# Performance work log

Measured on AMD Instinct MI355X. Metric: run time of the kernel, lower is better.

## Reference

```python
import jax, jax.numpy as jnp
import numpy as np

NEG_INF = -1e6  # d2l masked_softmax mask value

def setup_inputs() -> dict:
    key = jax.random.key(0)
    ks = jax.random.split(key, 6)
    B, Lq, Lk, dq, dv, H = 8, 256, 512, 256, 256, 64
    return {
        "queries": jax.random.normal(ks[0], (B, Lq, dq), jnp.float32),
        "keys": jax.random.normal(ks[1], (B, Lk, dq), jnp.float32),
        "values": jax.random.normal(ks[2], (B, Lk, dv), jnp.float32),
        "valid_lens": jax.random.randint(ks[3], (B,), 0, Lk),
        "W_q": jax.random.normal(ks[4], (H, dq), jnp.float32) * (dq ** -0.5),
        "W_k": jax.random.normal(ks[5], (H, dq), jnp.float32) * (dq ** -0.5),
        "w_v": jax.random.normal(jax.random.fold_in(key, 7), (H,), jnp.float32) * (H ** -0.5),
    }

def reference(queries, keys, values, valid_lens, W_q, W_k, w_v):
    # Project: [B,Lq,H], [B,Lk,H]
    q = jnp.einsum('bqd,hd->bqh', queries, W_q)
    k = jnp.einsum('bkd,hd->bkh', keys, W_k)
    # Broadcast-add + tanh: [B,Lq,Lk,H]
    features = jnp.tanh(q[:, :, None, :] + k[:, None, :, :])
    # Scalar projection -> scores [B,Lq,Lk]
    scores = jnp.einsum('bqkh,h->bqk', features, w_v)
    # masked_softmax over last axis with per-batch valid_lens
    Lk = keys.shape[1]
    mask = jnp.arange(Lk)[None, None, :] < valid_lens[:, None, None]
    scores = jnp.where(mask, scores, NEG_INF)
    attn = jax.nn.softmax(scores, axis=-1)
    # dropout p=0 (inference) -> identity; bmm with values
    return jnp.einsum('bqk,bkv->bqv', attn, values)
```

## Files before the change

### kernel.cpp

```cpp
#include <hip/hip_runtime.h>
#include <hip/hip_bf16.h>
#include <hip/hip_fp16.h>
#include <stdint.h>

#define NB 8
#define LQ 256
#define LK 512
#define NH 64
#define SCALE 2.8853900817779268f
#define L2E 1.4426950408889634f

#define QP_OFF   0
#define KP_OFF   131072
#define VBF_OFF  393216
#define PL_OFF   917504

extern "C" __device__ float __ocml_exp2_f32(float);
static __device__ __forceinline__ float fexp2(float x) {
#if __has_builtin(__builtin_amdgcn_exp2f)
  return __builtin_amdgcn_exp2f(x);
#else
  return __ocml_exp2_f32(x);
#endif
}
static __device__ __forceinline__ float frcp(float x) {
  return __builtin_amdgcn_rcpf(x);
}
static __device__ __forceinline__ uint16_t f2bf(float f) {
  uint32_t u = __float_as_uint(f);
  uint32_t r = (u + 0x7FFFu + ((u >> 16) & 1u)) >> 16;
  return (uint16_t)r;
}

typedef const __attribute__((address_space(1))) void* gas_ptr;
typedef __attribute__((address_space(3))) void* las_ptr;
static __device__ __forceinline__ void gload16(const void* g, void* l) {
  __builtin_amdgcn_global_load_lds((gas_ptr)g, (las_ptr)l, 16, 0, 0);
}

__global__ __launch_bounds__(256) void proj_kernel(
    const float* __restrict__ queries, const float* __restrict__ keys,
    const float* __restrict__ values,
    const float* __restrict__ Wq, const float* __restrict__ Wk,
    float* __restrict__ qp, float* __restrict__ kp, uint16_t* __restrict__ vbf)
{
  __shared__ float Wt[256][36];
  const int blk = blockIdx.x;
  const int t = threadIdx.x;

  if (blk >= 192) {
    int base = (blk - 192) * 16384 + t * 4;
#pragma unroll
    for (int it = 0; it < 16; ++it) {
      int idx = base + it * 1024;
      float4 v = *(const float4*)(values + idx);
      uint32_t lo = (uint32_t)f2bf(v.x) | ((uint32_t)f2bf(v.y) << 16);
      uint32_t hi = (uint32_t)f2bf(v.z) | ((uint32_t)f2bf(v.w) << 16);
      uint2 pk = {lo, hi};
      *(uint2*)(vbf + idx) = pk;
    }
    return;
  }

  const bool isQ = (blk < 64);
  const int sub = isQ ? blk : (blk - 64);
  const int tile = sub >> 1;
  const int hh = (sub & 1) * 32;
  const int rowbase = tile * 64;
  const float* __restrict__ X = isQ ? queries : keys;
  const float* __restrict__ W = isQ ? Wq : Wk;
  float* __restrict__ P = isQ ? qp : kp;

#pragma unroll 4
  for (int it = 0; it < 32; ++it) {
    Wt[t][it] = W[(hh + it) * 256 + t];
  }
  __syncthreads();

  const int ty = t >> 3;
  const int tx = t & 7;
  float a0x = 0.f, a0y = 0.f, a0z = 0.f, a0w = 0.f;
  float a1x = 0.f, a1y = 0.f, a1z = 0.f, a1w = 0.f;

  const float* xr0 = X + (size_t)(rowbase + ty * 2) * 256;
  const float* xr1 = xr0 + 256;

#pragma unroll 4
  for (int d4 = 0; d4 < 64; ++d4) {
    int d = d4 * 4;
    float4 x0 = *(const float4*)(xr0 + d);
    float4 x1 = *(const float4*)(xr1 + d);
    float4 w0 = *(const float4*)&Wt[d + 0][tx * 4];
    float4 w1 = *(const float4*)&Wt[d + 1][tx * 4];
    float4 w2 = *(const float4*)&Wt[d + 2][tx * 4];
    float4 w3 = *(const float4*)&Wt[d + 3][tx * 4];
#define STEP(XC, WD) \
    a0x = fmaf(x0.XC, WD.x, a0x); a0y = fmaf(x0.XC, WD.y, a0y); \
    a0z = fmaf(x0.XC, WD.z, a0z); a0w = fmaf(x0.XC, WD.w, a0w); \
    a1x = fmaf(x1.XC, WD.x, a1x); a1y = fmaf(x1.XC, WD.y, a1y); \
    a1z = fmaf(x1.XC, WD.z, a1z); a1w = fmaf(x1.XC, WD.w, a1w);
    STEP(x, w0) STEP(y, w1) STEP(z, w2) STEP(w, w3)
#undef STEP
  }

  {
    int row0 = rowbase + ty * 2;
    int h = hh + tx * 4;
    float4 o0 = {a0x * SCALE, a0y * SCALE, a0z * SCALE, a0w * SCALE};
    float4 o1 = {a1x * SCALE, a1y * SCALE, a1z * SCALE, a1w * SCALE};
    *(float4*)&P[(size_t)row0 * 64 + h] = o0;
    *(float4*)&P[(size_t)(row0 + 1) * 64 + h] = o1;
  }
}

__global__ __launch_bounds__(256) void attn_kernel(
    const float* __restrict__ qp, const float* __restrict__ kp,
    const uint16_t* __restrict__ vbf, const float* __restrict__ w_v,
    const int* __restrict__ valid_lens, float* __restrict__ out,
    float* __restrict__ pl, float* __restrict__ pacc, int nsplit)
{
  __shared__ float kTs[32][64];
  __shared__ uint16_t Vs[32][256];
  __shared__ float p_s[4][2][32];

  const int t = threadIdx.x;
  const int lane = t & 63;
  const int w = t >> 6;
  const int r2 = lane >> 5;
  const int kx = lane & 31;
  const int wg = blockIdx.x;
  const int b = wg & 7;
  const int qg = (wg >> 3) & 31;
  const int kh = wg >> 8;
  const int row = b * LQ + qg * 8 + w * 2 + r2;

  const int vl = valid_lens[b];
  const int n = (vl > 0) ? vl : LK;
  const int span = LK / nsplit;
  const int kstart = kh * span;
  int cnt = n - kstart;
  if (cnt > span) cnt = span;
  const int ntiles = (cnt > 0) ? ((cnt + 31) >> 5) : 0;

  if (ntiles == 0) {
    if (kx == 0) pl[row * nsplit + kh] = 0.f;
    float4 z = {0.f, 0.f, 0.f, 0.f};
    float* pa = pacc + ((size_t)(row * nsplit + kh)) * 256 + kx * 8;
    *(float4*)(pa + 0) = z;
    *(float4*)(pa + 4) = z;
    return;
  }

  const float* kpb = kp + (size_t)(b * LK) * 64;
  const char* vbc = (const char*)(vbf + (size_t)b * LK * 256);

#define STAGE(K0) do { \
    int i0 = w * 2; \
    int kjr0 = i0 * 4 + (lane >> 4); \
    int cph = lane & 15; \
    gload16(kpb + (size_t)((K0) + kjr0) * 64 + (cph ^ (kjr0 & 7)) * 4, \
            &kTs[i0 * 4][0]); \
    int kjr1 = kjr0 + 4; \
    gload16(kpb + (size_t)((K0) + kjr1) * 64 + (cph ^ (kjr1 & 7)) * 4, \
            &kTs[i0 * 4 + 4][0]); \
    const char* vsrc = vbc + (size_t)(K0) * 512 + (size_t)w * 4096 + lane * 16; \
    gload16(vsrc + 0 * 1024, &Vs[w * 8 + 0][0]); \
    gload16(vsrc + 1 * 1024, &Vs[w * 8 + 2][0]); \
    gload16(vsrc + 2 * 1024, &Vs[w * 8 + 4][0]); \
    gload16(vsrc + 3 * 1024, &Vs[w * 8 + 6][0]); \
  } while (0)

  STAGE(kstart);

  float W1 = 0.f;
#pragma unroll
  for (int g = 0; g < 16; ++g) {
    float4 wf = *(const float4*)(w_v + g * 4);
    W1 += (wf.x + wf.y) + (wf.z + wf.w);
  }
  const float W1L = W1 * L2E;

  float qv[64];
  {
    const float* qrow = qp + (size_t)row * 64;
#pragma unroll
    for (int i = 0; i < 16; ++i) {
      float4 v = *(const float4*)(qrow + i * 4);
      qv[i * 4 + 0] = v.x; qv[i * 4 + 1] = v.y;
      qv[i * 4 + 2] = v.z; qv[i * 4 + 3] = v.w;
    }
  }

  float l = 0.f;
  float acc[16];
#pragma unroll
  for (int i = 0; i < 16; ++i) acc[i] = 0.f;

  for (int tt = 0; tt < ntiles; ++tt) {
    const int k0 = kstart + tt * 32;
    asm volatile("s_waitcnt vmcnt(0)" ::: "memory");
    __builtin_amdgcn_sched_barrier(0);
    __builtin_amdgcn_s_barrier();
    __builtin_amdgcn_sched_barrier(0);
    __builtin_amdgcn_s_setprio(1);

    float r0 = 0.f, r1 = 0.f, r2a = 0.f, r3 = 0.f;
#pragma unroll
    for (int g = 0; g < 16; ++g) {
      float4 kf = *(const float4*)&kTs[kx][((g ^ (kx & 7)) << 2)];
      float4 wf = *(const float4*)(w_v + g * 4);
      r0  = fmaf(wf.x, frcp(1.f + fexp2(qv[g * 4 + 0] + kf.x)), r0);
      r1  = fmaf(wf.y, frcp(1.f + fexp2(qv[g * 4 + 1] + kf.y)), r1);
      r2a = fmaf(wf.z, frcp(1.f + fexp2(qv[g * 4 + 2] + kf.z)), r2a);
      r3  = fmaf(wf.w, frcp(1.f + fexp2(qv[g * 4 + 3] + kf.w)), r3);
    }
    float racc = (r0 + r1) + (r2a + r3);

    float pe = fexp2(fmaf(-SCALE, racc, W1L));
    int kg = k0 + kx;
    float p;
    if (vl == 0)      p = 1.f;
    else if (kg < n)  p = pe;
    else              p = 0.f;

    l += p;
    p_s[w][r2][kx] = p;

    const int c = kx;
#pragma unroll
    for (int i4 = 0; i4 < 4; ++i4) {
      float4 p0 = *(const float4*)&p_s[w][0][r2 * 16 + i4 * 4];
      float4 p1 = *(const float4*)&p_s[w][1][r2 * 16 + i4 * 4];
#pragma unroll
      for (int jj = 0; jj < 4; ++jj) {
        int kk = r2 * 16 + i4 * 4 + jj;
        uint4 vv = *(const uint4*)&Vs[kk][c * 8];
        float pj0 = (jj == 0) ? p0.x : (jj == 1) ? p0.y : (jj == 2) ? p0.z : p0.w;
        float pj1 = (jj == 0) ? p1.x : (jj == 1) ? p1.y : (jj == 2) ? p1.z : p1.w;
        float f0 = __uint_as_float(vv.x << 16);
        float f1 = __uint_as_float(vv.x & 0xFFFF0000u);
        float f2 = __uint_as_float(vv.y << 16);
        float f3 = __uint_as_float(vv.y & 0xFFFF0000u);
        float f4 = __uint_as_float(vv.z << 16);
        float f5 = __uint_as_float(vv.z & 0xFFFF0000u);
        float f6 = __uint_as_float(vv.w << 16);
        float f7 = __uint_as_float(vv.w & 0xFFFF0000u);
        acc[0] = fmaf(pj0, f0, acc[0]);   acc[8]  = fmaf(pj1, f0, acc[8]);
        acc[1] = fmaf(pj0, f1, acc[1]);   acc[9]  = fmaf(pj1, f1, acc[9]);
        acc[2] = fmaf(pj0, f2, acc[2]);   acc[10] = fmaf(pj1, f2, acc[10]);
        acc[3] = fmaf(pj0, f3, acc[3]);   acc[11] = fmaf(pj1, f3, acc[11]);
        acc[4] = fmaf(pj0, f4, acc[4]);   acc[12] = fmaf(pj1, f4, acc[12]);
        acc[5] = fmaf(pj0, f5, acc[5]);   acc[13] = fmaf(pj1, f5, acc[13]);
        acc[6] = fmaf(pj0, f6, acc[6]);   acc[14] = fmaf(pj1, f6, acc[14]);
        acc[7] = fmaf(pj0, f7, acc[7]);   acc[15] = fmaf(pj1, f7, acc[15]);
      }
    }
    __builtin_amdgcn_s_setprio(0);
    __builtin_amdgcn_sched_barrier(0);
    __builtin_amdgcn_s_barrier();
    if (tt + 1 < ntiles) STAGE(k0 + 32);
  }
#undef STAGE

#pragma unroll
  for (int i = 0; i < 16; ++i) acc[i] += __shfl_xor(acc[i], 32, 64);
#pragma unroll
  for (int s = 16; s; s >>= 1) l += __shfl_xor(l, s, 64);

  const float* accr = acc + r2 * 8;
  if (nsplit == 1) {
    float inv = 1.f / l;
    float4 o0 = {accr[0] * inv, accr[1] * inv, accr[2] * inv, accr[3] * inv};
    float4 o1 = {accr[4] * inv, accr[5] * inv, accr[6] * inv, accr[7] * inv};
    float* op = out + (size_t)row * 256 + kx * 8;
    *(float4*)(op + 0) = o0;
    *(float4*)(op + 4) = o1;
  } else {
    if (kx == 0) pl[row * nsplit + kh] = l;
    float* pa = pacc + ((size_t)(row * nsplit + kh)) * 256 + kx * 8;
    float4 a0 = {accr[0], accr[1], accr[2], accr[3]};
    float4 a1 = {accr[4], accr[5], accr[6], accr[7]};
    *(float4*)(pa + 0) = a0;
    *(float4*)(pa + 4) = a1;
  }
}

__global__ __launch_bounds__(256) void merge_kernel(
    const float* __restrict__ pl, const float* __restrict__ pacc,
    float* __restrict__ out, int nsplit)
{
  const int t = threadIdx.x;
  const int row = blockIdx.x * 8 + (t >> 5);
  const int d8 = t & 31;

  float L = 0.f;
  float o[8];
#pragma unroll
  for (int i = 0; i < 8; ++i) o[i] = 0.f;

  for (int kh = 0; kh < nsplit; ++kh) {
    L += pl[row * nsplit + kh];
    const float* pa = pacc + ((size_t)(row * nsplit + kh)) * 256 + d8 * 8;
    float4 a0 = *(const float4*)(pa + 0);
    float4 a1 = *(const float4*)(pa + 4);
    o[0] += a0.x; o[1] += a0.y; o[2] += a0.z; o[3] += a0.w;
    o[4] += a1.x; o[5] += a1.y; o[6] += a1.z; o[7] += a1.w;
  }
  float inv = 1.f / L;
  float4 o0 = {o[0] * inv, o[1] * inv, o[2] * inv, o[3] * inv};
  float4 o1 = {o[4] * inv, o[5] * inv, o[6] * inv, o[7] * inv};
  float* op = out + (size_t)row * 256 + d8 * 8;
  *(float4*)(op + 0) = o0;
  *(float4*)(op + 4) = o1;
}

extern "C" void kernel_launch(void* const* d_in, const int* in_sizes, int n_in,
                              void* d_out, int out_size, void* d_ws, size_t ws_size,
                              hipStream_t stream) {
  const float* queries    = (const float*)d_in[0];
  const float* keys       = (const float*)d_in[1];
  const float* values     = (const float*)d_in[2];
  const int*   valid_lens = (const int*)d_in[3];
  const float* Wq         = (const float*)d_in[4];
  const float* Wk         = (const float*)d_in[5];
  const float* w_v        = (const float*)d_in[6];
  float* out = (float*)d_out;

  float* ws = (float*)d_ws;
  float* qp  = ws + QP_OFF;
  float* kp  = ws + KP_OFF;
  uint16_t* vbf = (uint16_t*)(ws + VBF_OFF);
  float* pl  = ws + PL_OFF;

  int nsplit;
  if      (ws_size >= (size_t)PL_OFF * 4 + 2048u * 4 * 4 + 2048u * 4 * 1024) nsplit = 4;
  else if (ws_size >= (size_t)PL_OFF * 4 + 2048u * 2 * 4 + 2048u * 2 * 1024) nsplit = 2;
  else nsplit = 1;
  float* pacc = pl + (size_t)2048 * nsplit;

  hipLaunchKernelGGL(proj_kernel, dim3(256), dim3(256), 0, stream,
                     queries, keys, values, Wq, Wk, qp, kp, vbf);
  hipLaunchKernelGGL(attn_kernel, dim3(nsplit * 256), dim3(256), 0, stream,
                     qp, kp, vbf, w_v, valid_lens, out, pl, pacc, nsplit);
  if (nsplit > 1) {
    hipLaunchKernelGGL(merge_kernel, dim3(256), dim3(256), 0, stream,
                       pl, pacc, out, nsplit);
  }
}
```

Measured before the change: 44.34 us.

## Move query rows to LDS, halve accumulators, raise occupancy and allow 8-way split

Each lane no longer keeps the 64-float projected query row in registers. The block stages its 8 query rows in shared memory once and reads a float4 per step of the score loop. The PV accumulation changes so each lane handles its own query row over all 32 keys with 8 accumulators. That removes the cross-half shuffle reduction and halves the accumulator registers. A launch bound of 8 blocks per CU and an 8-way key split, used when the workspace is large enough, add occupancy and parallelism, at the cost of extra LDS reads of V and query data plus a heavier merge pass.

```diff
diff --git a/kernel.cpp b/kernel.cpp
--- a/kernel.cpp
+++ b/kernel.cpp
@@ -113,7 +113,7 @@
   }
 }
 
-__global__ __launch_bounds__(256) void attn_kernel(
+__global__ __launch_bounds__(256, 8) void attn_kernel(
     const float* __restrict__ qp, const float* __restrict__ kp,
     const uint16_t* __restrict__ vbf, const float* __restrict__ w_v,
     const int* __restrict__ valid_lens, float* __restrict__ out,
@@ -121,6 +121,7 @@
 {
   __shared__ float kTs[32][64];
   __shared__ uint16_t Vs[32][256];
+  __shared__ float q_s[4][2][64];
   __shared__ float p_s[4][2][32];
 
   const int t = threadIdx.x;
@@ -172,6 +173,11 @@
 
   STAGE(kstart);
 
+  {
+    const float2* qsrc = (const float2*)(qp + (size_t)(b * LQ + qg * 8) * 64);
+    ((float2*)q_s)[t] = qsrc[t];
+  }
+
   float W1 = 0.f;
 #pragma unroll
   for (int g = 0; g < 16; ++g) {
@@ -180,21 +186,10 @@
   }
   const float W1L = W1 * L2E;
 
-  float qv[64];
-  {
-    const float* qrow = qp + (size_t)row * 64;
-#pragma unroll
-    for (int i = 0; i < 16; ++i) {
-      float4 v = *(const float4*)(qrow + i * 4);
-      qv[i * 4 + 0] = v.x; qv[i * 4 + 1] = v.y;
-      qv[i * 4 + 2] = v.z; qv[i * 4 + 3] = v.w;
-    }
-  }
-
   float l = 0.f;
-  float acc[16];
-#pragma unroll
-  for (int i = 0; i < 16; ++i) acc[i] = 0.f;
+  float acc[8];
+#pragma unroll
+  for (int i = 0; i < 8; ++i) acc[i] = 0.f;
 
   for (int tt = 0; tt < ntiles; ++tt) {
     const int k0 = kstart + tt * 32;
@@ -208,11 +203,12 @@
 #pragma unroll
     for (int g = 0; g < 16; ++g) {
       float4 kf = *(const float4*)&kTs[kx][((g ^ (kx & 7)) << 2)];
+      float4 qf = *(const float4*)&q_s[w][r2][g * 4];
       float4 wf = *(const float4*)(w_v + g * 4);
-      r0  = fmaf(wf.x, frcp(1.f + fexp2(qv[g * 4 + 0] + kf.x)), r0);
-      r1  = fmaf(wf.y, frcp(1.f + fexp2(qv[g * 4 + 1] + kf.y)), r1);
-      r2a = fmaf(wf.z, frcp(1.f + fexp2(qv[g * 4 + 2] + kf.z)), r2a);
-      r3  = fmaf(wf.w, frcp(1.f + fexp2(qv[g * 4 + 3] + kf.w)), r3);
+      r0  = fmaf(wf.x, frcp(1.f + fexp2(qf.x + kf.x)), r0);
+      r1  = fmaf(wf.y, frcp(1.f + fexp2(qf.y + kf.y)), r1);
+      r2a = fmaf(wf.z, frcp(1.f + fexp2(qf.z + kf.z)), r2a);
+      r3  = fmaf(wf.w, frcp(1.f + fexp2(qf.w + kf.w)), r3);
     }
     float racc = (r0 + r1) + (r2a + r3);
 
@@ -228,15 +224,13 @@
 
     const int c = kx;
 #pragma unroll
-    for (int i4 = 0; i4 < 4; ++i4) {
-      float4 p0 = *(const float4*)&p_s[w][0][r2 * 16 + i4 * 4];
-      float4 p1 = *(const float4*)&p_s[w][1][r2 * 16 + i4 * 4];
+    for (int kk4 = 0; kk4 < 8; ++kk4) {
+      float4 pf = *(const float4*)&p_s[w][r2][kk4 * 4];
 #pragma unroll
       for (int jj = 0; jj < 4; ++jj) {
-        int kk = r2 * 16 + i4 * 4 + jj;
+        int kk = kk4 * 4 + jj;
         uint4 vv = *(const uint4*)&Vs[kk][c * 8];
-        float pj0 = (jj == 0) ? p0.x : (jj == 1) ? p0.y : (jj == 2) ? p0.z : p0.w;
-        float pj1 = (jj == 0) ? p1.x : (jj == 1) ? p1.y : (jj == 2) ? p1.z : p1.w;
+        float pj = (jj == 0) ? pf.x : (jj == 1) ? pf.y : (jj == 2) ? pf.z : pf.w;
         float f0 = __uint_as_float(vv.x << 16);
         float f1 = __uint_as_float(vv.x & 0xFFFF0000u);
         float f2 = __uint_as_float(vv.y << 16);
@@ -245,14 +239,14 @@
         float f5 = __uint_as_float(vv.z & 0xFFFF0000u);
         float f6 = __uint_as_float(vv.w << 16);
         float f7 = __uint_as_float(vv.w & 0xFFFF0000u);
-        acc[0] = fmaf(pj0, f0, acc[0]);   acc[8]  = fmaf(pj1, f0, acc[8]);
-        acc[1] = fmaf(pj0, f1, acc[1]);   acc[9]  = fmaf(pj1, f1, acc[9]);
-        acc[2] = fmaf(pj0, f2, acc[2]);   acc[10] = fmaf(pj1, f2, acc[10]);
-        acc[3] = fmaf(pj0, f3, acc[3]);   acc[11] = fmaf(pj1, f3, acc[11]);
-        acc[4] = fmaf(pj0, f4, acc[4]);   acc[12] = fmaf(pj1, f4, acc[12]);
-        acc[5] = fmaf(pj0, f5, acc[5]);   acc[13] = fmaf(pj1, f5, acc[13]);
-        acc[6] = fmaf(pj0, f6, acc[6]);   acc[14] = fmaf(pj1, f6, acc[14]);
-        acc[7] = fmaf(pj0, f7, acc[7]);   acc[15] = fmaf(pj1, f7, acc[15]);
+        acc[0] = fmaf(pj, f0, acc[0]);
+        acc[1] = fmaf(pj, f1, acc[1]);
+        acc[2] = fmaf(pj, f2, acc[2]);
+        acc[3] = fmaf(pj, f3, acc[3]);
+        acc[4] = fmaf(pj, f4, acc[4]);
+        acc[5] = fmaf(pj, f5, acc[5]);
+        acc[6] = fmaf(pj, f6, acc[6]);
+        acc[7] = fmaf(pj, f7, acc[7]);
       }
     }
     __builtin_amdgcn_s_setprio(0);
@@ -263,23 +257,20 @@
 #undef STAGE
 
 #pragma unroll
-  for (int i = 0; i < 16; ++i) acc[i] += __shfl_xor(acc[i], 32, 64);
-#pragma unroll
   for (int s = 16; s; s >>= 1) l += __shfl_xor(l, s, 64);
 
-  const float* accr = acc + r2 * 8;
   if (nsplit == 1) {
     float inv = 1.f / l;
-    float4 o0 = {accr[0] * inv, accr[1] * inv, accr[2] * inv, accr[3] * inv};
-    float4 o1 = {accr[4] * inv, accr[5] * inv, accr[6] * inv, accr[7] * inv};
+    float4 o0 = {acc[0] * inv, acc[1] * inv, acc[2] * inv, acc[3] * inv};
+    float4 o1 = {acc[4] * inv, acc[5] * inv, acc[6] * inv, acc[7] * inv};
     float* op = out + (size_t)row * 256 + kx * 8;
     *(float4*)(op + 0) = o0;
     *(float4*)(op + 4) = o1;
   } else {
     if (kx == 0) pl[row * nsplit + kh] = l;
     float* pa = pacc + ((size_t)(row * nsplit + kh)) * 256 + kx * 8;
-    float4 a0 = {accr[0], accr[1], accr[2], accr[3]};
-    float4 a1 = {accr[4], accr[5], accr[6], accr[7]};
+    float4 a0 = {acc[0], acc[1], acc[2], acc[3]};
+    float4 a1 = {acc[4], acc[5], acc[6], acc[7]};
     *(float4*)(pa + 0) = a0;
     *(float4*)(pa + 4) = a1;
   }
@@ -333,7 +324,8 @@
   float* pl  = ws + PL_OFF;
 
   int nsplit;
-  if      (ws_size >= (size_t)PL_OFF * 4 + 2048u * 4 * 4 + 2048u * 4 * 1024) nsplit = 4;
+  if      (ws_size >= (size_t)PL_OFF * 4 + 2048u * 8 * 4 + 2048u * 8 * 1024) nsplit = 8;
+  else if (ws_size >= (size_t)PL_OFF * 4 + 2048u * 4 * 4 + 2048u * 4 * 1024) nsplit = 4;
   else if (ws_size >= (size_t)PL_OFF * 4 + 2048u * 2 * 4 + 2048u * 2 * 1024) nsplit = 2;
   else nsplit = 1;
   float* pacc = pl + (size_t)2048 * nsplit;
```

After: 51.78 us. 16.8% more time.

## Give each lane its own key and loop over two query rows per wave

Applied to the files above, without the earlier changes.

The score phase now maps one key per lane over a 64-key tile, and each lane evaluates both query rows of the wave in sequence, with the query rows staged in shared memory instead of held in 64 registers. Key and value tiles double to 64 rows. The split-K count drops from 4 to 2, so the split-K partial writes and merge traffic shrink. The aim is to free registers and to use all 64 lanes in the tanh phase. The cost is fewer workgroups (512 instead of 1024), larger shared memory per block, and extra LDS reads of the query rows.

```diff
diff --git a/kernel.cpp b/kernel.cpp
--- a/kernel.cpp
+++ b/kernel.cpp
@@ -119,20 +119,22 @@
     const int* __restrict__ valid_lens, float* __restrict__ out,
     float* __restrict__ pl, float* __restrict__ pacc, int nsplit)
 {
-  __shared__ float kTs[32][64];
-  __shared__ uint16_t Vs[32][256];
-  __shared__ float p_s[4][2][32];
+  __shared__ float kTs[64][64];
+  __shared__ uint16_t Vs[64][256];
+  __shared__ float q_s[4][2][64];
+  __shared__ float p_s[4][2][64];
 
   const int t = threadIdx.x;
   const int lane = t & 63;
   const int w = t >> 6;
-  const int r2 = lane >> 5;
-  const int kx = lane & 31;
+  const int half = lane >> 5;
+  const int c = lane & 31;
+  const int kj = lane;
   const int wg = blockIdx.x;
   const int b = wg & 7;
   const int qg = (wg >> 3) & 31;
   const int kh = wg >> 8;
-  const int row = b * LQ + qg * 8 + w * 2 + r2;
+  const int row0 = b * LQ + qg * 8 + w * 2;
 
   const int vl = valid_lens[b];
   const int n = (vl > 0) ? vl : LK;
@@ -140,12 +142,12 @@
   const int kstart = kh * span;
   int cnt = n - kstart;
   if (cnt > span) cnt = span;
-  const int ntiles = (cnt > 0) ? ((cnt + 31) >> 5) : 0;
+  const int ntiles = (cnt > 0) ? ((cnt + 63) >> 6) : 0;
 
   if (ntiles == 0) {
-    if (kx == 0) pl[row * nsplit + kh] = 0.f;
+    if (c == 0) pl[(row0 + half) * nsplit + kh] = 0.f;
     float4 z = {0.f, 0.f, 0.f, 0.f};
-    float* pa = pacc + ((size_t)(row * nsplit + kh)) * 256 + kx * 8;
+    float* pa = pacc + ((size_t)((row0 + half) * nsplit + kh)) * 256 + c * 8;
     *(float4*)(pa + 0) = z;
     *(float4*)(pa + 4) = z;
     return;
@@ -155,22 +157,37 @@
   const char* vbc = (const char*)(vbf + (size_t)b * LK * 256);
 
 #define STAGE(K0) do { \
-    int i0 = w * 2; \
-    int kjr0 = i0 * 4 + (lane >> 4); \
     int cph = lane & 15; \
-    gload16(kpb + (size_t)((K0) + kjr0) * 64 + (cph ^ (kjr0 & 7)) * 4, \
-            &kTs[i0 * 4][0]); \
-    int kjr1 = kjr0 + 4; \
-    gload16(kpb + (size_t)((K0) + kjr1) * 64 + (cph ^ (kjr1 & 7)) * 4, \
-            &kTs[i0 * 4 + 4][0]); \
-    const char* vsrc = vbc + (size_t)(K0) * 512 + (size_t)w * 4096 + lane * 16; \
-    gload16(vsrc + 0 * 1024, &Vs[w * 8 + 0][0]); \
-    gload16(vsrc + 1 * 1024, &Vs[w * 8 + 2][0]); \
-    gload16(vsrc + 2 * 1024, &Vs[w * 8 + 4][0]); \
-    gload16(vsrc + 3 * 1024, &Vs[w * 8 + 6][0]); \
+    int kr0 = w * 16 + (lane >> 4); \
+    gload16(kpb + (size_t)((K0) + kr0) * 64 + ((cph ^ (kr0 & 7)) << 2), \
+            &kTs[w * 16][0]); \
+    int kr1 = kr0 + 4; \
+    gload16(kpb + (size_t)((K0) + kr1) * 64 + ((cph ^ (kr1 & 7)) << 2), \
+            &kTs[w * 16 + 4][0]); \
+    int kr2 = kr0 + 8; \
+    gload16(kpb + (size_t)((K0) + kr2) * 64 + ((cph ^ (kr2 & 7)) << 2), \
+            &kTs[w * 16 + 8][0]); \
+    int kr3 = kr0 + 12; \
+    gload16(kpb + (size_t)((K0) + kr3) * 64 + ((cph ^ (kr3 & 7)) << 2), \
+            &kTs[w * 16 + 12][0]); \
+    const char* vsrc = vbc + (size_t)((K0) + w * 16) * 512 + lane * 16; \
+    gload16(vsrc + 0 * 1024, &Vs[w * 16 +  0][0]); \
+    gload16(vsrc + 1 * 1024, &Vs[w * 16 +  2][0]); \
+    gload16(vsrc + 2 * 1024, &Vs[w * 16 +  4][0]); \
+    gload16(vsrc + 3 * 1024, &Vs[w * 16 +  6][0]); \
+    gload16(vsrc + 4 * 1024, &Vs[w * 16 +  8][0]); \
+    gload16(vsrc + 5 * 1024, &Vs[w * 16 + 10][0]); \
+    gload16(vsrc + 6 * 1024, &Vs[w * 16 + 12][0]); \
+    gload16(vsrc + 7 * 1024, &Vs[w * 16 + 14][0]); \
   } while (0)
 
   STAGE(kstart);
+
+  {
+    const float2* qsrc = (const float2*)(qp + (size_t)row0 * 64 - (size_t)(w * 128) + (size_t)(w * 128));
+    ((float2*)q_s)[t] = ((const float2*)(qp + (size_t)(b * LQ + qg * 8) * 64))[t];
+    (void)qsrc;
+  }
 
   float W1 = 0.f;
 #pragma unroll
@@ -180,60 +197,52 @@
   }
   const float W1L = W1 * L2E;
 
-  float qv[64];
-  {
-    const float* qrow = qp + (size_t)row * 64;
-#pragma unroll
-    for (int i = 0; i < 16; ++i) {
-      float4 v = *(const float4*)(qrow + i * 4);
-      qv[i * 4 + 0] = v.x; qv[i * 4 + 1] = v.y;
-      qv[i * 4 + 2] = v.z; qv[i * 4 + 3] = v.w;
-    }
-  }
-
-  float l = 0.f;
+  float l0 = 0.f, l1 = 0.f;
   float acc[16];
 #pragma unroll
   for (int i = 0; i < 16; ++i) acc[i] = 0.f;
 
   for (int tt = 0; tt < ntiles; ++tt) {
-    const int k0 = kstart + tt * 32;
+    const int k0 = kstart + tt * 64;
     asm volatile("s_waitcnt vmcnt(0)" ::: "memory");
     __builtin_amdgcn_sched_barrier(0);
     __builtin_amdgcn_s_barrier();
     __builtin_amdgcn_sched_barrier(0);
     __builtin_amdgcn_s_setprio(1);
 
-    float r0 = 0.f, r1 = 0.f, r2a = 0.f, r3 = 0.f;
-#pragma unroll
-    for (int g = 0; g < 16; ++g) {
-      float4 kf = *(const float4*)&kTs[kx][((g ^ (kx & 7)) << 2)];
-      float4 wf = *(const float4*)(w_v + g * 4);
-      r0  = fmaf(wf.x, frcp(1.f + fexp2(qv[g * 4 + 0] + kf.x)), r0);
-      r1  = fmaf(wf.y, frcp(1.f + fexp2(qv[g * 4 + 1] + kf.y)), r1);
-      r2a = fmaf(wf.z, frcp(1.f + fexp2(qv[g * 4 + 2] + kf.z)), r2a);
-      r3  = fmaf(wf.w, frcp(1.f + fexp2(qv[g * 4 + 3] + kf.w)), r3);
+    const int kg = k0 + kj;
+    const bool inb = (kg < n);
+
+#pragma unroll
+    for (int r = 0; r < 2; ++r) {
+      float r0 = 0.f, r1 = 0.f, r2a = 0.f, r3 = 0.f;
+#pragma unroll
+      for (int g = 0; g < 16; ++g) {
+        float4 kf = *(const float4*)&kTs[kj][((g ^ (kj & 7)) << 2)];
+        float4 qf = *(const float4*)&q_s[w][r][g * 4];
+        float4 wf = *(const float4*)(w_v + g * 4);
+        r0  = fmaf(wf.x, frcp(1.f + fexp2(qf.x + kf.x)), r0);
+        r1  = fmaf(wf.y, frcp(1.f + fexp2(qf.y + kf.y)), r1);
+        r2a = fmaf(wf.z, frcp(1.f + fexp2(qf.z + kf.z)), r2a);
+        r3  = fmaf(wf.w, frcp(1.f + fexp2(qf.w + kf.w)), r3);
+      }
+      float racc = (r0 + r1) + (r2a + r3);
+      float pe = fexp2(fmaf(-SCALE, racc, W1L));
+      float p;
+      if (vl == 0)   p = 1.f;
+      else if (inb)  p = pe;
+      else           p = 0.f;
+      if (r == 0) l0 += p; else l1 += p;
+      p_s[w][r][kj] = p;
     }
-    float racc = (r0 + r1) + (r2a + r3);
-
-    float pe = fexp2(fmaf(-SCALE, racc, W1L));
-    int kg = k0 + kx;
-    float p;
-    if (vl == 0)      p = 1.f;
-    else if (kg < n)  p = pe;
-    else              p = 0.f;
-
-    l += p;
-    p_s[w][r2][kx] = p;
-
-    const int c = kx;
-#pragma unroll
-    for (int i4 = 0; i4 < 4; ++i4) {
-      float4 p0 = *(const float4*)&p_s[w][0][r2 * 16 + i4 * 4];
-      float4 p1 = *(const float4*)&p_s[w][1][r2 * 16 + i4 * 4];
+
+#pragma unroll
+    for (int kk4 = 0; kk4 < 8; ++kk4) {
+      float4 p0 = *(const float4*)&p_s[w][0][half * 32 + kk4 * 4];
+      float4 p1 = *(const float4*)&p_s[w][1][half * 32 + kk4 * 4];
 #pragma unroll
       for (int jj = 0; jj < 4; ++jj) {
-        int kk = r2 * 16 + i4 * 4 + jj;
+        int kk = half * 32 + kk4 * 4 + jj;
         uint4 vv = *(const uint4*)&Vs[kk][c * 8];
         float pj0 = (jj == 0) ? p0.x : (jj == 1) ? p0.y : (jj == 2) ? p0.z : p0.w;
         float pj1 = (jj == 0) ? p1.x : (jj == 1) ? p1.y : (jj == 2) ? p1.z : p1.w;
@@ -258,26 +267,28 @@
     __builtin_amdgcn_s_setprio(0);
     __builtin_amdgcn_sched_barrier(0);
     __builtin_amdgcn_s_barrier();
-    if (tt + 1 < ntiles) STAGE(k0 + 32);
+    if (tt + 1 < ntiles) STAGE(k0 + 64);
   }
 #undef STAGE
 
 #pragma unroll
   for (int i = 0; i < 16; ++i) acc[i] += __shfl_xor(acc[i], 32, 64);
 #pragma unroll
-  for (int s = 16; s; s >>= 1) l += __shfl_xor(l, s, 64);
-
-  const float* accr = acc + r2 * 8;
+  for (int s = 32; s; s >>= 1) { l0 += __shfl_xor(l0, s, 64); l1 += __shfl_xor(l1, s, 64); }
+
+  const float lsel = half ? l1 : l0;
+  const float* accr = acc + half * 8;
+  const int row = row0 + half;
   if (nsplit == 1) {
-    float inv = 1.f / l;
+    float inv = 1.f / lsel;
     float4 o0 = {accr[0] * inv, accr[1] * inv, accr[2] * inv, accr[3] * inv};
     float4 o1 = {accr[4] * inv, accr[5] * inv, accr[6] * inv, accr[7] * inv};
-    float* op = out + (size_t)row * 256 + kx * 8;
+    float* op = out + (size_t)row * 256 + c * 8;
     *(float4*)(op + 0) = o0;
     *(float4*)(op + 4) = o1;
   } else {
-    if (kx == 0) pl[row * nsplit + kh] = l;
-    float* pa = pacc + ((size_t)(row * nsplit + kh)) * 256 + kx * 8;
+    if (c == 0) pl[row * nsplit + kh] = lsel;
+    float* pa = pacc + ((size_t)(row * nsplit + kh)) * 256 + c * 8;
     float4 a0 = {accr[0], accr[1], accr[2], accr[3]};
     float4 a1 = {accr[4], accr[5], accr[6], accr[7]};
     *(float4*)(pa + 0) = a0;
@@ -333,8 +344,7 @@
   float* pl  = ws + PL_OFF;
 
   int nsplit;
-  if      (ws_size >= (size_t)PL_OFF * 4 + 2048u * 4 * 4 + 2048u * 4 * 1024) nsplit = 4;
-  else if (ws_size >= (size_t)PL_OFF * 4 + 2048u * 2 * 4 + 2048u * 2 * 1024) nsplit = 2;
+  if      (ws_size >= (size_t)PL_OFF * 4 + 2048u * 2 * 4 + 2048u * 2 * 1024) nsplit = 2;
   else nsplit = 1;
   float* pacc = pl + (size_t)2048 * nsplit;
 
```

Measured after the change: 51.42 us. 1.16x slower.
